# Performance work log

Measured on AMD Instinct MI355X. Metric: run time of the kernel, lower is better.

Reference implementation:

```python
import jax, jax.numpy as jnp
import numpy as np

ALPHA = 2.0   # surrogate.atan(alpha=2)
BETA = 0.9    # membrane decay
THR = 1.0     # spike threshold

@jax.custom_vjp
def atan_spike(x):
    # Heaviside forward, atan surrogate backward (snntorch convention)
    return (x > 0).astype(x.dtype)

def _atan_fwd(x):
    return atan_spike(x), x

def _atan_bwd(x, g):
    return (g * (ALPHA / 2.0) / (1.0 + (jnp.pi / 2.0 * ALPHA * x) ** 2),)

atan_spike.defvjp(_atan_fwd, _atan_bwd)


def setup_inputs() -> dict:
    key = jax.random.key(0)
    ks = jax.random.split(key, 7)
    B, T, I = 128, 128, 1024
    dims = [2048, 2048, 1024]
    x = jax.random.normal(ks[0], (B, T, I), dtype=jnp.float32)
    fan_ins = [I, dims[0], dims[1]]
    W0 = jax.random.normal(ks[1], (dims[0], fan_ins[0]), dtype=jnp.float32) / np.sqrt(fan_ins[0])
    b0 = jax.random.normal(ks[2], (dims[0],), dtype=jnp.float32) * 0.01
    W1 = jax.random.normal(ks[3], (dims[1], fan_ins[1]), dtype=jnp.float32) / np.sqrt(fan_ins[1])
    b1 = jax.random.normal(ks[4], (dims[1],), dtype=jnp.float32) * 0.01
    W2 = jax.random.normal(ks[5], (dims[2], fan_ins[2]), dtype=jnp.float32) / np.sqrt(fan_ins[2])
    b2 = jax.random.normal(ks[6], (dims[2],), dtype=jnp.float32) * 0.01
    return {"x": x, "W0": W0, "b0": b0, "W1": W1, "b1": b1, "W2": W2, "b2": b2}


def reference(x, W0, b0, W1, b1, W2, b2):
    params = ((W0, b0), (W1, b1), (W2, b2))
    B = x.shape[0]
    dims = [W0.shape[0], W1.shape[0], W2.shape[0]]
    v0 = tuple(jnp.zeros((B, d), x.dtype) for d in dims)

    def step(volts, x_t):
        h = x_t
        new_volts = []
        v = None
        for (W, b), vi in zip(params, volts):
            cur = h @ W.T + b            # [B, d]
            v = BETA * vi + cur           # leaky integration
            spk = atan_spike(v - THR)     # threshold
            v = v - spk * THR             # reset by subtraction
            new_volts.append(v)
            h = spk
        return tuple(new_volts), (h, v)

    xT = jnp.swapaxes(x, 0, 1)            # [T, B, I]
    _, (spikes, volts) = jax.lax.scan(step, v0, xT)
    # [T, B, D] -> [B, T, D]
    return jnp.swapaxes(spikes, 0, 1), jnp.swapaxes(volts, 0, 1)
```

## Files before the change

kernel.cpp:

```cpp
#include <hip/hip_runtime.h>
#include <stdint.h>


#define TT   128
#define NB   128
#define DD2  1024

#define SPK0_OFF 0u
#define SPK1_OFF (128u*128u*64u)
#define PART_OFF (2u*128u*128u*64u)
#define NHELP    192u
#define FLG_OFF  (PART_OFF + NHELP*4096u)
#define NFLG     1536u
#define WS_NEED_BYTES ((size_t)(FLG_OFF + NFLG) * 4u)

__device__ __forceinline__ void wait_ge(uint32_t* p, uint32_t tgt){
  while (__hip_atomic_load(p, __ATOMIC_ACQUIRE, __HIP_MEMORY_SCOPE_AGENT) < tgt)
    __builtin_amdgcn_s_sleep(1);
}

__device__ __forceinline__ int fswz(int k){
  return (k & 16) | ((k ^ (k >> 3)) & 12);
}

__global__ void sentinel_kernel(float* o){ o[0] = 42.0f; }

__global__ __launch_bounds__(256, 2) void snn_kernel(
    const float* __restrict__ x,
    const float* __restrict__ W0, const float* __restrict__ b0,
    const float* __restrict__ W1, const float* __restrict__ b1,
    const float* __restrict__ W2, const float* __restrict__ b2,
    float* __restrict__ out, uint32_t* __restrict__ ws)
{
  __shared__ __align__(16) float lA[128][68];
  __shared__ __align__(16) float lB[32][132];
  __shared__ uint32_t lBits[64];

  const int tid = threadIdx.x;
  const int tm  = tid & 15;
  const int tn  = tid >> 4;
  const int bid = blockIdx.x;

  uint32_t* spikes0  = ws + SPK0_OFF;
  uint32_t* spikes1  = ws + SPK1_OFF;
  float*    partials = (float*)(ws + PART_OFF);
  uint32_t* flg   = ws + FLG_OFF;
  uint32_t* pflag = flg;
  uint32_t* oflag = flg + 512;
  uint32_t* done0 = flg + 1024;
  uint32_t* done1 = flg + 1280;

  int group, kp, tl, m0, n0, K, hslot;
  const float *Wl, *bl;
  const uint32_t* spkIn; uint32_t* spkOut;
  uint32_t *dIn, *dOut;
  if (bid < 128) {
    group=0; kp=0; tl=bid;
    m0=(tl>>6)*64; n0=(tl&63)*32; K=1024; Wl=W0; bl=b0;
    spkIn=nullptr; spkOut=spikes0; dIn=nullptr; dOut=done0 + (m0>>6)*128; hslot=-1;
  } else if (bid < 384) {
    group=1; int rel=bid-128; kp=rel&1; tl=rel>>1;
    m0=(tl>>6)*64; n0=(tl&63)*32; K=2048; Wl=W1; bl=b1;
    spkIn=spikes0; spkOut=spikes1;
    dIn=done0 + (m0>>6)*128; dOut=done1 + (m0>>6)*128; hslot=tl;
  } else {
    group=2; int rel=bid-384; kp=rel&1; tl=rel>>1;
    m0=(tl>>5)*64; n0=(tl&31)*32; K=2048; Wl=W2; bl=b2;
    spkIn=spikes1; spkOut=nullptr;
    dIn=done1 + (m0>>6)*128; dOut=nullptr; hslot=128+tl;
  }
  const bool owner = (kp == 0);
  const int  K0    = kp * 1024;

  const float bias0 = bl[n0 + tn*2 + 0];
  const float bias1 = bl[n0 + tn*2 + 1];

  float vst[4][2];
  #pragma unroll
  for (int r = 0; r < 4; ++r) { vst[r][0] = 0.f; vst[r][1] = 0.f; }

  for (int t = 0; t < TT; ++t) {
    if (dIn) {
      if (tid == 0) wait_ge(&dIn[t], 64u);
      __syncthreads();
    }

    float acc2[2][4][2];
    #pragma unroll
    for (int p = 0; p < 2; ++p) {
      #pragma unroll
      for (int r = 0; r < 4; ++r) { acc2[p][r][0] = 0.f; acc2[p][r][1] = 0.f; }

      #pragma unroll 1
      for (int ch = 0; ch < 4; ++ch) {
        const int kb = K0 + p*512 + ch*128;

        #pragma unroll
        for (int it = 0; it < 4; ++it) {
          int idx = tid + it*256;
          int nrow = idx >> 5, kq = idx & 31;
          float4 w = *(const float4*)(Wl + (size_t)(n0+nrow)*K + kb + kq*4);
          *(float4*)&lB[nrow][kq*4] = w;
        }

        if (group == 0) {
          #pragma unroll
          for (int it = 0; it < 8; ++it) {
            int idx = tid + it*256;
            int mrow = idx >> 5, kq = idx & 31;
            float4 v = *(const float4*)(x + ((size_t)(m0+mrow)*TT + t)*1024 + kb + kq*4);
            int k0 = kq*4;
            lA[k0+0][mrow ^ fswz(k0+0)] = v.x;
            lA[k0+1][mrow ^ fswz(k0+1)] = v.y;
            lA[k0+2][mrow ^ fswz(k0+2)] = v.z;
            lA[k0+3][mrow ^ fswz(k0+3)] = v.w;
          }
        } else {
          const int mq   = tid & 15;
          const int sub  = tid >> 4;
          const int wsub = sub & 3;
          const int kq8  = sub >> 2;
          const size_t rb = ((size_t)t*NB + m0 + mq*4)*64 + (kb>>5) + wsub;
          uint32_t w0 = __hip_atomic_load(&spkIn[rb      ], __ATOMIC_RELAXED, __HIP_MEMORY_SCOPE_AGENT);
          uint32_t w1 = __hip_atomic_load(&spkIn[rb +  64], __ATOMIC_RELAXED, __HIP_MEMORY_SCOPE_AGENT);
          uint32_t w2 = __hip_atomic_load(&spkIn[rb + 128], __ATOMIC_RELAXED, __HIP_MEMORY_SCOPE_AGENT);
          uint32_t w3 = __hip_atomic_load(&spkIn[rb + 192], __ATOMIC_RELAXED, __HIP_MEMORY_SCOPE_AGENT);
          const int kloc = wsub*32 + kq8*8;
          #pragma unroll
          for (int i = 0; i < 8; ++i) {
            int k  = kloc + i;
            int sh = k & 31;
            float4 f;
            f.x = ((w0 >> sh) & 1u) ? 1.0f : 0.0f;
            f.y = ((w1 >> sh) & 1u) ? 1.0f : 0.0f;
            f.z = ((w2 >> sh) & 1u) ? 1.0f : 0.0f;
            f.w = ((w3 >> sh) & 1u) ? 1.0f : 0.0f;
            *(float4*)&lA[k][(mq*4) ^ fswz(k)] = f;
          }
        }
        __syncthreads();

        const float* bp0 = &lB[tn*2    ][0];
        const float* bp1 = &lB[tn*2 + 1][0];
        #pragma unroll 4
        for (int k4 = 0; k4 < 32; ++k4) {
          const int kbase = k4*4;
          const int col = (tm*4) ^ fswz(kbase);
          #pragma unroll
          for (int u = 0; u < 4; ++u) {
            const float4 a  = *(const float4*)&lA[kbase+u][col];
            const float bv0 = bp0[kbase+u];
            const float bv1 = bp1[kbase+u];
            acc2[p][0][0] = __builtin_fmaf(a.x, bv0, acc2[p][0][0]);
            acc2[p][1][0] = __builtin_fmaf(a.y, bv0, acc2[p][1][0]);
            acc2[p][2][0] = __builtin_fmaf(a.z, bv0, acc2[p][2][0]);
            acc2[p][3][0] = __builtin_fmaf(a.w, bv0, acc2[p][3][0]);
            acc2[p][0][1] = __builtin_fmaf(a.x, bv1, acc2[p][0][1]);
            acc2[p][1][1] = __builtin_fmaf(a.y, bv1, acc2[p][1][1]);
            acc2[p][2][1] = __builtin_fmaf(a.z, bv1, acc2[p][2][1]);
            acc2[p][3][1] = __builtin_fmaf(a.w, bv1, acc2[p][3][1]);
          }
        }
        __syncthreads();
      }
    }

    if (!owner) {
      if (t >= 1) { if (tid == 0) wait_ge(&oflag[bid-1], (uint32_t)t); __syncthreads(); }
      uint64_t* pb = (uint64_t*)(partials + (size_t)hslot*4096) + tid*8;
      #pragma unroll
      for (int h = 0; h < 2; ++h)
        #pragma unroll
        for (int r = 0; r < 4; ++r) {
          union { float f[2]; uint64_t u; } cv;
          cv.f[0] = acc2[h][r][0]; cv.f[1] = acc2[h][r][1];
          __hip_atomic_store(&pb[h*4+r], cv.u, __ATOMIC_RELAXED, __HIP_MEMORY_SCOPE_AGENT);
        }
      __syncthreads();
      if (tid == 0) __hip_atomic_store(&pflag[bid], (uint32_t)(t+1), __ATOMIC_RELEASE, __HIP_MEMORY_SCOPE_AGENT);
      continue;
    }

    float acc[4][2];
    #pragma unroll
    for (int r = 0; r < 4; ++r) {
      acc[r][0] = __fadd_rn(acc2[0][r][0], acc2[1][r][0]);
      acc[r][1] = __fadd_rn(acc2[0][r][1], acc2[1][r][1]);
    }

    if (hslot >= 0) {
      if (tid == 0) wait_ge(&pflag[bid+1], (uint32_t)(t+1));
      __syncthreads();
      uint64_t* pb = (uint64_t*)(partials + (size_t)hslot*4096) + tid*8;
      #pragma unroll
      for (int h = 0; h < 2; ++h)
        #pragma unroll
        for (int r = 0; r < 4; ++r) {
          union { uint64_t u; float f[2]; } cv;
          cv.u = __hip_atomic_load(&pb[h*4+r], __ATOMIC_RELAXED, __HIP_MEMORY_SCOPE_AGENT);
          acc[r][0] = __fadd_rn(acc[r][0], cv.f[0]);
          acc[r][1] = __fadd_rn(acc[r][1], cv.f[1]);
        }
      __syncthreads();
      if (tid == 0) __hip_atomic_store(&oflag[bid], (uint32_t)(t+1), __ATOMIC_RELEASE, __HIP_MEMORY_SCOPE_AGENT);
    }

    if (group < 2) { if (tid < 64) lBits[tid] = 0; __syncthreads(); }

    float sv[4][2], vv8[4][2];
    #pragma unroll
    for (int r = 0; r < 4; ++r) {
      uint32_t msk = 0;
      #pragma unroll
      for (int c = 0; c < 2; ++c) {
        float cur = __fadd_rn(acc[r][c], c ? bias1 : bias0);
        float vv  = __fadd_rn(__fmul_rn(0.9f, vst[r][c]), cur);
        float s   = (vv > 1.0f) ? 1.0f : 0.0f;
        vv = __fsub_rn(vv, s);
        vst[r][c] = vv;
        sv[r][c] = s; vv8[r][c] = vv;
        msk |= (s != 0.f) ? (1u << (tn*2 + c)) : 0u;
      }
      if (group < 2 && msk) atomicOr(&lBits[tm*4 + r], msk);
    }

    if (group == 2) {
      #pragma unroll
      for (int r = 0; r < 4; ++r) {
        size_t o  = ((size_t)(m0 + tm*4 + r)*TT + t)*DD2 + n0 + tn*2;
        *(float2*)(out + o)  = make_float2(sv[r][0], sv[r][1]);
        size_t ov = (size_t)NB*TT*DD2 + o;
        *(float2*)(out + ov) = make_float2(vv8[r][0], vv8[r][1]);
      }
    } else {
      __syncthreads();
      if (tid < 64)
        __hip_atomic_store(&spkOut[((size_t)t*NB + m0 + tid)*64 + (n0>>5)],
                           lBits[tid], __ATOMIC_RELAXED, __HIP_MEMORY_SCOPE_AGENT);
      __syncthreads();
      if (tid == 0) __hip_atomic_fetch_add(&dOut[t], 1u, __ATOMIC_RELEASE, __HIP_MEMORY_SCOPE_AGENT);
    }
  }
}

extern "C" void kernel_launch(void* const* d_in, const int* in_sizes, int n_in,
                              void* d_out, int out_size, void* d_ws, size_t ws_size,
                              hipStream_t stream) {
  (void)in_sizes; (void)n_in; (void)out_size;
  float* outf = (float*)d_out;
  if (ws_size < WS_NEED_BYTES) {
    sentinel_kernel<<<1, 1, 0, stream>>>(outf);
    return;
  }
  const float* x  = (const float*)d_in[0];
  const float* W0 = (const float*)d_in[1];
  const float* b0 = (const float*)d_in[2];
  const float* W1 = (const float*)d_in[3];
  const float* b1 = (const float*)d_in[4];
  const float* W2 = (const float*)d_in[5];
  const float* b2 = (const float*)d_in[6];
  uint32_t* ws = (uint32_t*)d_ws;

  hipMemsetAsync(ws + FLG_OFF, 0, NFLG * sizeof(uint32_t), stream);

  snn_kernel<<<512, 256, 0, stream>>>(x, W0, b0, W1, b1, W2, b2, outf, ws);
}
```

Before: 7.599 ms.

## Double-buffer LDS tiles with register prefetch, one barrier per chunk

Halves the K chunk from 128 to 64 and double-buffers the A/B shared-memory tiles. The next chunk's weights, inputs or spike words are prefetched into registers while the current chunk is computed, and the second barrier per chunk is dropped. B values are read as float4 vectors instead of scalars. The aim is to hide global-load latency behind the FMA loop and cut barrier count. The cost is more registers under launch_bounds(256,2) and a hand-placed waitcnt/barrier sequence that has to stay correct.

```diff
diff --git a/kernel.cpp b/kernel.cpp
--- a/kernel.cpp
+++ b/kernel.cpp
@@ -32,8 +32,8 @@
     const float* __restrict__ W2, const float* __restrict__ b2,
     float* __restrict__ out, uint32_t* __restrict__ ws)
 {
-  __shared__ __align__(16) float lA[128][68];
-  __shared__ __align__(16) float lB[32][132];
+  __shared__ __align__(16) float lA[2][64][68];
+  __shared__ __align__(16) float lB[2][32][68];
   __shared__ uint32_t lBits[64];
 
   const int tid = threadIdx.x;
@@ -79,6 +79,31 @@
   #pragma unroll
   for (int r = 0; r < 4; ++r) { vst[r][0] = 0.f; vst[r][1] = 0.f; }
 
+  float4   ra[4];
+  float4   rb[2];
+  uint32_t rw[4];
+
+  const int s_sub = tid >> 4;
+  const int s_kq  = tid & 15;
+
+#define LOAD_REGS(KB) do {                                                     \
+    const int kb_ = (KB);                                                      \
+    _Pragma("unroll")                                                          \
+    for (int it = 0; it < 2; ++it)                                             \
+      rb[it] = *(const float4*)(Wl + (size_t)(n0 + s_sub + it*16)*K + kb_ + s_kq*4); \
+    if (group == 0) {                                                          \
+      _Pragma("unroll")                                                        \
+      for (int it = 0; it < 4; ++it)                                           \
+        ra[it] = *(const float4*)(x + ((size_t)(m0 + s_sub + it*16)*TT + t)*1024 + kb_ + s_kq*4); \
+    } else {                                                                   \
+      const size_t base_ = ((size_t)t*NB + m0 + s_kq*4)*64 + (kb_>>5) + (s_sub>>3); \
+      _Pragma("unroll")                                                        \
+      for (int j = 0; j < 4; ++j)                                              \
+        rw[j] = __hip_atomic_load(&spkIn[base_ + (size_t)j*64],                \
+                                  __ATOMIC_RELAXED, __HIP_MEMORY_SCOPE_AGENT); \
+    }                                                                          \
+  } while (0)
+
   for (int t = 0; t < TT; ++t) {
     if (dIn) {
       if (tid == 0) wait_ge(&dIn[t], 64u);
@@ -87,70 +112,65 @@
 
     float acc2[2][4][2];
     #pragma unroll
+    for (int p = 0; p < 2; ++p)
+      #pragma unroll
+      for (int r = 0; r < 4; ++r) { acc2[p][r][0] = 0.f; acc2[p][r][1] = 0.f; }
+
+    LOAD_REGS(K0);
+
+    #pragma unroll
     for (int p = 0; p < 2; ++p) {
-      #pragma unroll
-      for (int r = 0; r < 4; ++r) { acc2[p][r][0] = 0.f; acc2[p][r][1] = 0.f; }
-
-      #pragma unroll 1
-      for (int ch = 0; ch < 4; ++ch) {
-        const int kb = K0 + p*512 + ch*128;
+      #pragma unroll 2
+      for (int ch = 0; ch < 8; ++ch) {
+        const int buf = ch & 1;
+        float (*cA)[68] = lA[buf];
+        float (*cB)[68] = lB[buf];
 
         #pragma unroll
-        for (int it = 0; it < 4; ++it) {
-          int idx = tid + it*256;
-          int nrow = idx >> 5, kq = idx & 31;
-          float4 w = *(const float4*)(Wl + (size_t)(n0+nrow)*K + kb + kq*4);
-          *(float4*)&lB[nrow][kq*4] = w;
-        }
-
+        for (int it = 0; it < 2; ++it)
+          *(float4*)&cB[s_sub + it*16][s_kq*4] = rb[it];
         if (group == 0) {
+          const int k0 = s_kq*4, sw = fswz(k0);
           #pragma unroll
-          for (int it = 0; it < 8; ++it) {
-            int idx = tid + it*256;
-            int mrow = idx >> 5, kq = idx & 31;
-            float4 v = *(const float4*)(x + ((size_t)(m0+mrow)*TT + t)*1024 + kb + kq*4);
-            int k0 = kq*4;
-            lA[k0+0][mrow ^ fswz(k0+0)] = v.x;
-            lA[k0+1][mrow ^ fswz(k0+1)] = v.y;
-            lA[k0+2][mrow ^ fswz(k0+2)] = v.z;
-            lA[k0+3][mrow ^ fswz(k0+3)] = v.w;
+          for (int it = 0; it < 4; ++it) {
+            const int col = (s_sub + it*16) ^ sw;
+            cA[k0+0][col] = ra[it].x; cA[k0+1][col] = ra[it].y;
+            cA[k0+2][col] = ra[it].z; cA[k0+3][col] = ra[it].w;
           }
         } else {
-          const int mq   = tid & 15;
-          const int sub  = tid >> 4;
-          const int wsub = sub & 3;
-          const int kq8  = sub >> 2;
-          const size_t rb = ((size_t)t*NB + m0 + mq*4)*64 + (kb>>5) + wsub;
-          uint32_t w0 = __hip_atomic_load(&spkIn[rb      ], __ATOMIC_RELAXED, __HIP_MEMORY_SCOPE_AGENT);
-          uint32_t w1 = __hip_atomic_load(&spkIn[rb +  64], __ATOMIC_RELAXED, __HIP_MEMORY_SCOPE_AGENT);
-          uint32_t w2 = __hip_atomic_load(&spkIn[rb + 128], __ATOMIC_RELAXED, __HIP_MEMORY_SCOPE_AGENT);
-          uint32_t w3 = __hip_atomic_load(&spkIn[rb + 192], __ATOMIC_RELAXED, __HIP_MEMORY_SCOPE_AGENT);
-          const int kloc = wsub*32 + kq8*8;
           #pragma unroll
-          for (int i = 0; i < 8; ++i) {
-            int k  = kloc + i;
-            int sh = k & 31;
+          for (int i = 0; i < 4; ++i) {
+            const int k  = s_sub*4 + i;
+            const int sh = k & 31;
             float4 f;
-            f.x = ((w0 >> sh) & 1u) ? 1.0f : 0.0f;
-            f.y = ((w1 >> sh) & 1u) ? 1.0f : 0.0f;
-            f.z = ((w2 >> sh) & 1u) ? 1.0f : 0.0f;
-            f.w = ((w3 >> sh) & 1u) ? 1.0f : 0.0f;
-            *(float4*)&lA[k][(mq*4) ^ fswz(k)] = f;
+            f.x = ((rw[0] >> sh) & 1u) ? 1.0f : 0.0f;
+            f.y = ((rw[1] >> sh) & 1u) ? 1.0f : 0.0f;
+            f.z = ((rw[2] >> sh) & 1u) ? 1.0f : 0.0f;
+            f.w = ((rw[3] >> sh) & 1u) ? 1.0f : 0.0f;
+            *(float4*)&cA[k][(s_kq*4) ^ fswz(k)] = f;
           }
         }
-        __syncthreads();
-
-        const float* bp0 = &lB[tn*2    ][0];
-        const float* bp1 = &lB[tn*2 + 1][0];
+
+        if (ch < 7)        LOAD_REGS(K0 + p*512 + (ch+1)*64);
+        else if (p == 0)   LOAD_REGS(K0 + 512);
+
+        __builtin_amdgcn_sched_barrier(0);
+        asm volatile("s_waitcnt lgkmcnt(0)" ::: "memory");
+        __builtin_amdgcn_s_barrier();
+        __builtin_amdgcn_sched_barrier(0);
+
         #pragma unroll 4
-        for (int k4 = 0; k4 < 32; ++k4) {
+        for (int k4 = 0; k4 < 16; ++k4) {
           const int kbase = k4*4;
-          const int col = (tm*4) ^ fswz(kbase);
+          const int sw = fswz(kbase);
+          const float* pa = &cA[kbase][(tm*4) ^ sw];
+          const float4 b0 = *(const float4*)&cB[tn*2    ][kbase];
+          const float4 b1 = *(const float4*)&cB[tn*2 + 1][kbase];
           #pragma unroll
           for (int u = 0; u < 4; ++u) {
-            const float4 a  = *(const float4*)&lA[kbase+u][col];
-            const float bv0 = bp0[kbase+u];
-            const float bv1 = bp1[kbase+u];
+            const float4 a  = *(const float4*)(pa + u*68);
+            const float bv0 = (u==0) ? b0.x : (u==1) ? b0.y : (u==2) ? b0.z : b0.w;
+            const float bv1 = (u==0) ? b1.x : (u==1) ? b1.y : (u==2) ? b1.z : b1.w;
             acc2[p][0][0] = __builtin_fmaf(a.x, bv0, acc2[p][0][0]);
             acc2[p][1][0] = __builtin_fmaf(a.y, bv0, acc2[p][1][0]);
             acc2[p][2][0] = __builtin_fmaf(a.z, bv0, acc2[p][2][0]);
@@ -161,7 +181,6 @@
             acc2[p][3][1] = __builtin_fmaf(a.w, bv1, acc2[p][3][1]);
           }
         }
-        __syncthreads();
       }
     }
 
@@ -241,6 +260,7 @@
       if (tid == 0) __hip_atomic_fetch_add(&dOut[t], 1u, __ATOMIC_RELEASE, __HIP_MEMORY_SCOPE_AGENT);
     }
   }
+#undef LOAD_REGS
 }
 
 extern "C" void kernel_launch(void* const* d_in, const int* in_sizes, int n_in,
```

Result: slower. 10.09 ms (+32.7%).

## Merge split-K block pairs into 512-thread blocks with LDS partial reduction

Applied to the files above, without the earlier changes.

Each pair of split-K blocks for layers 1 and 2 becomes one 512-thread block. The two halves exchange partial sums through shared memory and a barrier, instead of through global partial buffers guarded by per-block flags. Layer-0 blocks now each handle two tiles, and the done-counter targets are adjusted to match the new block counts. The inner loop also reads the weight tile as float4 instead of scalar loads. The cost is doubled shared memory per block, so fewer blocks fit on each CU.

```diff
diff --git a/kernel.cpp b/kernel.cpp
--- a/kernel.cpp
+++ b/kernel.cpp
@@ -19,58 +19,56 @@
     __builtin_amdgcn_s_sleep(1);
 }
 
-__device__ __forceinline__ int fswz(int k){
+__device__ __forceinline__ constexpr int fswz(int k){
   return (k & 16) | ((k ^ (k >> 3)) & 12);
 }
 
 __global__ void sentinel_kernel(float* o){ o[0] = 42.0f; }
 
-__global__ __launch_bounds__(256, 2) void snn_kernel(
+__global__ __launch_bounds__(512, 2) void snn_kernel(
     const float* __restrict__ x,
     const float* __restrict__ W0, const float* __restrict__ b0,
     const float* __restrict__ W1, const float* __restrict__ b1,
     const float* __restrict__ W2, const float* __restrict__ b2,
     float* __restrict__ out, uint32_t* __restrict__ ws)
 {
-  __shared__ __align__(16) float lA[128][68];
-  __shared__ __align__(16) float lB[32][132];
-  __shared__ uint32_t lBits[64];
-
-  const int tid = threadIdx.x;
-  const int tm  = tid & 15;
-  const int tn  = tid >> 4;
-  const int bid = blockIdx.x;
-
-  uint32_t* spikes0  = ws + SPK0_OFF;
-  uint32_t* spikes1  = ws + SPK1_OFF;
-  float*    partials = (float*)(ws + PART_OFF);
+  __shared__ __align__(16) float lA[2][128][68];
+  __shared__ __align__(16) float lB[2][32][132];
+  __shared__ uint32_t lBits2[2][64];
+
+  const int tid  = threadIdx.x;
+  const int h    = tid >> 8;
+  const int t256 = tid & 255;
+  const int tm   = t256 & 15;
+  const int tn   = t256 >> 4;
+  const int bid  = blockIdx.x;
+
+  uint32_t* spikes0 = ws + SPK0_OFF;
+  uint32_t* spikes1 = ws + SPK1_OFF;
   uint32_t* flg   = ws + FLG_OFF;
-  uint32_t* pflag = flg;
-  uint32_t* oflag = flg + 512;
   uint32_t* done0 = flg + 1024;
   uint32_t* done1 = flg + 1280;
 
-  int group, kp, tl, m0, n0, K, hslot;
+  int group, tl, m0, n0, K, K0, dTgt;
   const float *Wl, *bl;
   const uint32_t* spkIn; uint32_t* spkOut;
   uint32_t *dIn, *dOut;
-  if (bid < 128) {
-    group=0; kp=0; tl=bid;
-    m0=(tl>>6)*64; n0=(tl&63)*32; K=1024; Wl=W0; bl=b0;
-    spkIn=nullptr; spkOut=spikes0; dIn=nullptr; dOut=done0 + (m0>>6)*128; hslot=-1;
-  } else if (bid < 384) {
-    group=1; int rel=bid-128; kp=rel&1; tl=rel>>1;
-    m0=(tl>>6)*64; n0=(tl&63)*32; K=2048; Wl=W1; bl=b1;
+  if (bid < 64) {
+    group=0; tl=bid*2+h;
+    m0=(tl>>6)*64; n0=(tl&63)*32; K=1024; K0=0; Wl=W0; bl=b0;
+    spkIn=nullptr; spkOut=spikes0; dIn=nullptr; dOut=done0+(m0>>6)*128; dTgt=0;
+  } else if (bid < 192) {
+    group=1; tl=bid-64;
+    m0=(tl>>6)*64; n0=(tl&63)*32; K=2048; K0=h*1024; Wl=W1; bl=b1;
     spkIn=spikes0; spkOut=spikes1;
-    dIn=done0 + (m0>>6)*128; dOut=done1 + (m0>>6)*128; hslot=tl;
+    dIn=done0+(m0>>6)*128; dOut=done1+(m0>>6)*128; dTgt=32;
   } else {
-    group=2; int rel=bid-384; kp=rel&1; tl=rel>>1;
-    m0=(tl>>5)*64; n0=(tl&31)*32; K=2048; Wl=W2; bl=b2;
+    group=2; tl=bid-192;
+    m0=(tl>>5)*64; n0=(tl&31)*32; K=2048; K0=h*1024; Wl=W2; bl=b2;
     spkIn=spikes1; spkOut=nullptr;
-    dIn=done1 + (m0>>6)*128; dOut=nullptr; hslot=128+tl;
+    dIn=done1+(m0>>6)*128; dOut=nullptr; dTgt=64;
   }
-  const bool owner = (kp == 0);
-  const int  K0    = kp * 1024;
+  const bool own = (group == 0) || (h == 0);
 
   const float bias0 = bl[n0 + tn*2 + 0];
   const float bias1 = bl[n0 + tn*2 + 1];
@@ -79,78 +77,85 @@
   #pragma unroll
   for (int r = 0; r < 4; ++r) { vst[r][0] = 0.f; vst[r][1] = 0.f; }
 
+  const int e_mq   = t256 & 15;
+  const int e_sub  = t256 >> 4;
+  const int e_wsub = e_sub & 3;
+  const int e_kq8  = e_sub >> 2;
+  const int e_kloc = e_wsub*32 + e_kq8*8;
+
+  float (*cA)[68]  = lA[h];
+  float (*cB)[132] = lB[h];
+
   for (int t = 0; t < TT; ++t) {
     if (dIn) {
-      if (tid == 0) wait_ge(&dIn[t], 64u);
+      if (tid == 0) wait_ge(&dIn[t], (uint32_t)dTgt);
       __syncthreads();
     }
 
     float acc2[2][4][2];
     #pragma unroll
-    for (int p = 0; p < 2; ++p) {
+    for (int p = 0; p < 2; ++p)
       #pragma unroll
       for (int r = 0; r < 4; ++r) { acc2[p][r][0] = 0.f; acc2[p][r][1] = 0.f; }
 
+    #pragma unroll
+    for (int p = 0; p < 2; ++p) {
       #pragma unroll 1
       for (int ch = 0; ch < 4; ++ch) {
         const int kb = K0 + p*512 + ch*128;
 
         #pragma unroll
         for (int it = 0; it < 4; ++it) {
-          int idx = tid + it*256;
+          int idx = t256 + it*256;
           int nrow = idx >> 5, kq = idx & 31;
           float4 w = *(const float4*)(Wl + (size_t)(n0+nrow)*K + kb + kq*4);
-          *(float4*)&lB[nrow][kq*4] = w;
+          *(float4*)&cB[nrow][kq*4] = w;
         }
 
         if (group == 0) {
           #pragma unroll
           for (int it = 0; it < 8; ++it) {
-            int idx = tid + it*256;
+            int idx = t256 + it*256;
             int mrow = idx >> 5, kq = idx & 31;
             float4 v = *(const float4*)(x + ((size_t)(m0+mrow)*TT + t)*1024 + kb + kq*4);
             int k0 = kq*4;
-            lA[k0+0][mrow ^ fswz(k0+0)] = v.x;
-            lA[k0+1][mrow ^ fswz(k0+1)] = v.y;
-            lA[k0+2][mrow ^ fswz(k0+2)] = v.z;
-            lA[k0+3][mrow ^ fswz(k0+3)] = v.w;
+            lA[h][k0+0][mrow ^ fswz(k0+0)] = v.x;
+            lA[h][k0+1][mrow ^ fswz(k0+1)] = v.y;
+            lA[h][k0+2][mrow ^ fswz(k0+2)] = v.z;
+            lA[h][k0+3][mrow ^ fswz(k0+3)] = v.w;
           }
         } else {
-          const int mq   = tid & 15;
-          const int sub  = tid >> 4;
-          const int wsub = sub & 3;
-          const int kq8  = sub >> 2;
-          const size_t rb = ((size_t)t*NB + m0 + mq*4)*64 + (kb>>5) + wsub;
-          uint32_t w0 = __hip_atomic_load(&spkIn[rb      ], __ATOMIC_RELAXED, __HIP_MEMORY_SCOPE_AGENT);
-          uint32_t w1 = __hip_atomic_load(&spkIn[rb +  64], __ATOMIC_RELAXED, __HIP_MEMORY_SCOPE_AGENT);
-          uint32_t w2 = __hip_atomic_load(&spkIn[rb + 128], __ATOMIC_RELAXED, __HIP_MEMORY_SCOPE_AGENT);
-          uint32_t w3 = __hip_atomic_load(&spkIn[rb + 192], __ATOMIC_RELAXED, __HIP_MEMORY_SCOPE_AGENT);
-          const int kloc = wsub*32 + kq8*8;
+          const size_t rbase = ((size_t)t*NB + m0 + e_mq*4)*64 + (kb>>5) + e_wsub;
+          uint32_t w0 = __hip_atomic_load(&spkIn[rbase      ], __ATOMIC_RELAXED, __HIP_MEMORY_SCOPE_AGENT);
+          uint32_t w1 = __hip_atomic_load(&spkIn[rbase +  64], __ATOMIC_RELAXED, __HIP_MEMORY_SCOPE_AGENT);
+          uint32_t w2 = __hip_atomic_load(&spkIn[rbase + 128], __ATOMIC_RELAXED, __HIP_MEMORY_SCOPE_AGENT);
+          uint32_t w3 = __hip_atomic_load(&spkIn[rbase + 192], __ATOMIC_RELAXED, __HIP_MEMORY_SCOPE_AGENT);
           #pragma unroll
           for (int i = 0; i < 8; ++i) {
-            int k  = kloc + i;
+            int k  = e_kloc + i;
             int sh = k & 31;
             float4 f;
             f.x = ((w0 >> sh) & 1u) ? 1.0f : 0.0f;
             f.y = ((w1 >> sh) & 1u) ? 1.0f : 0.0f;
             f.z = ((w2 >> sh) & 1u) ? 1.0f : 0.0f;
             f.w = ((w3 >> sh) & 1u) ? 1.0f : 0.0f;
-            *(float4*)&lA[k][(mq*4) ^ fswz(k)] = f;
+            *(float4*)&cA[k][(e_mq*4) ^ fswz(k)] = f;
           }
         }
         __syncthreads();
 
-        const float* bp0 = &lB[tn*2    ][0];
-        const float* bp1 = &lB[tn*2 + 1][0];
         #pragma unroll 4
         for (int k4 = 0; k4 < 32; ++k4) {
           const int kbase = k4*4;
-          const int col = (tm*4) ^ fswz(kbase);
+          const int sw = fswz(kbase);
+          const float* pa = &cA[kbase][(tm*4) ^ sw];
+          const float4 b0v = *(const float4*)&cB[tn*2    ][kbase];
+          const float4 b1v = *(const float4*)&cB[tn*2 + 1][kbase];
           #pragma unroll
           for (int u = 0; u < 4; ++u) {
-            const float4 a  = *(const float4*)&lA[kbase+u][col];
-            const float bv0 = bp0[kbase+u];
-            const float bv1 = bp1[kbase+u];
+            const float4 a  = *(const float4*)(pa + u*68);
+            const float bv0 = (u==0) ? b0v.x : (u==1) ? b0v.y : (u==2) ? b0v.z : b0v.w;
+            const float bv1 = (u==0) ? b1v.x : (u==1) ? b1v.y : (u==2) ? b1v.z : b1v.w;
             acc2[p][0][0] = __builtin_fmaf(a.x, bv0, acc2[p][0][0]);
             acc2[p][1][0] = __builtin_fmaf(a.y, bv0, acc2[p][1][0]);
             acc2[p][2][0] = __builtin_fmaf(a.z, bv0, acc2[p][2][0]);
@@ -165,22 +170,6 @@
       }
     }
 
-    if (!owner) {
-      if (t >= 1) { if (tid == 0) wait_ge(&oflag[bid-1], (uint32_t)t); __syncthreads(); }
-      uint64_t* pb = (uint64_t*)(partials + (size_t)hslot*4096) + tid*8;
-      #pragma unroll
-      for (int h = 0; h < 2; ++h)
-        #pragma unroll
-        for (int r = 0; r < 4; ++r) {
-          union { float f[2]; uint64_t u; } cv;
-          cv.f[0] = acc2[h][r][0]; cv.f[1] = acc2[h][r][1];
-          __hip_atomic_store(&pb[h*4+r], cv.u, __ATOMIC_RELAXED, __HIP_MEMORY_SCOPE_AGENT);
-        }
-      __syncthreads();
-      if (tid == 0) __hip_atomic_store(&pflag[bid], (uint32_t)(t+1), __ATOMIC_RELEASE, __HIP_MEMORY_SCOPE_AGENT);
-      continue;
-    }
-
     float acc[4][2];
     #pragma unroll
     for (int r = 0; r < 4; ++r) {
@@ -188,55 +177,64 @@
       acc[r][1] = __fadd_rn(acc2[0][r][1], acc2[1][r][1]);
     }
 
-    if (hslot >= 0) {
-      if (tid == 0) wait_ge(&pflag[bid+1], (uint32_t)(t+1));
-      __syncthreads();
-      uint64_t* pb = (uint64_t*)(partials + (size_t)hslot*4096) + tid*8;
-      #pragma unroll
-      for (int h = 0; h < 2; ++h)
-        #pragma unroll
-        for (int r = 0; r < 4; ++r) {
-          union { uint64_t u; float f[2]; } cv;
-          cv.u = __hip_atomic_load(&pb[h*4+r], __ATOMIC_RELAXED, __HIP_MEMORY_SCOPE_AGENT);
-          acc[r][0] = __fadd_rn(acc[r][0], cv.f[0]);
-          acc[r][1] = __fadd_rn(acc[r][1], cv.f[1]);
-        }
-      __syncthreads();
-      if (tid == 0) __hip_atomic_store(&oflag[bid], (uint32_t)(t+1), __ATOMIC_RELEASE, __HIP_MEMORY_SCOPE_AGENT);
-    }
-
-    if (group < 2) { if (tid < 64) lBits[tid] = 0; __syncthreads(); }
-
-    float sv[4][2], vv8[4][2];
-    #pragma unroll
-    for (int r = 0; r < 4; ++r) {
-      uint32_t msk = 0;
-      #pragma unroll
-      for (int c = 0; c < 2; ++c) {
-        float cur = __fadd_rn(acc[r][c], c ? bias1 : bias0);
-        float vv  = __fadd_rn(__fmul_rn(0.9f, vst[r][c]), cur);
-        float s   = (vv > 1.0f) ? 1.0f : 0.0f;
-        vv = __fsub_rn(vv, s);
-        vst[r][c] = vv;
-        sv[r][c] = s; vv8[r][c] = vv;
-        msk |= (s != 0.f) ? (1u << (tn*2 + c)) : 0u;
-      }
-      if (group < 2 && msk) atomicOr(&lBits[tm*4 + r], msk);
-    }
-
-    if (group == 2) {
+    if (group != 0) {
+      float* ex = &lA[1][0][0];
+      if (h == 1) {
+        #pragma unroll
+        for (int q = 0; q < 4; ++q) {
+          const int hh = q >> 1, rb = (q & 1) * 2;
+          *(float4*)&ex[t256*16 + q*4] = make_float4(
+              acc2[hh][rb+0][0], acc2[hh][rb+0][1],
+              acc2[hh][rb+1][0], acc2[hh][rb+1][1]);
+        }
+      }
+      __syncthreads();
+      if (h == 0) {
+        #pragma unroll
+        for (int hh = 0; hh < 2; ++hh)
+          #pragma unroll
+          for (int r = 0; r < 4; ++r) {
+            acc[r][0] = __fadd_rn(acc[r][0], ex[t256*16 + hh*8 + r*2 + 0]);
+            acc[r][1] = __fadd_rn(acc[r][1], ex[t256*16 + hh*8 + r*2 + 1]);
+          }
+      }
+    }
+
+    if (group < 2) { if (t256 < 64) lBits2[h][t256] = 0; __syncthreads(); }
+
+    if (own) {
+      float sv[4][2], vv8[4][2];
       #pragma unroll
       for (int r = 0; r < 4; ++r) {
-        size_t o  = ((size_t)(m0 + tm*4 + r)*TT + t)*DD2 + n0 + tn*2;
-        *(float2*)(out + o)  = make_float2(sv[r][0], sv[r][1]);
-        size_t ov = (size_t)NB*TT*DD2 + o;
-        *(float2*)(out + ov) = make_float2(vv8[r][0], vv8[r][1]);
-      }
-    } else {
-      __syncthreads();
-      if (tid < 64)
-        __hip_atomic_store(&spkOut[((size_t)t*NB + m0 + tid)*64 + (n0>>5)],
-                           lBits[tid], __ATOMIC_RELAXED, __HIP_MEMORY_SCOPE_AGENT);
+        uint32_t msk = 0;
+        #pragma unroll
+        for (int c = 0; c < 2; ++c) {
+          float cur = __fadd_rn(acc[r][c], c ? bias1 : bias0);
+          float vv  = __fadd_rn(__fmul_rn(0.9f, vst[r][c]), cur);
+          float s   = (vv > 1.0f) ? 1.0f : 0.0f;
+          vv = __fsub_rn(vv, s);
+          vst[r][c] = vv;
+          sv[r][c] = s; vv8[r][c] = vv;
+          msk |= (s != 0.f) ? (1u << (tn*2 + c)) : 0u;
+        }
+        if (group < 2 && msk) atomicOr(&lBits2[h][tm*4 + r], msk);
+      }
+      if (group == 2) {
+        #pragma unroll
+        for (int r = 0; r < 4; ++r) {
+          size_t o  = ((size_t)(m0 + tm*4 + r)*TT + t)*DD2 + n0 + tn*2;
+          *(float2*)(out + o)  = make_float2(sv[r][0], sv[r][1]);
+          size_t ov = (size_t)NB*TT*DD2 + o;
+          *(float2*)(out + ov) = make_float2(vv8[r][0], vv8[r][1]);
+        }
+      }
+    }
+
+    if (group < 2) {
+      __syncthreads();
+      if (own && t256 < 64)
+        __hip_atomic_store(&spkOut[((size_t)t*NB + m0 + t256)*64 + (n0>>5)],
+                           lBits2[h][t256], __ATOMIC_RELAXED, __HIP_MEMORY_SCOPE_AGENT);
       __syncthreads();
       if (tid == 0) __hip_atomic_fetch_add(&dOut[t], 1u, __ATOMIC_RELEASE, __HIP_MEMORY_SCOPE_AGENT);
     }
@@ -263,5 +261,5 @@
 
   hipMemsetAsync(ws + FLG_OFF, 0, NFLG * sizeof(uint32_t), stream);
 
-  snn_kernel<<<512, 256, 0, stream>>>(x, W0, b0, W1, b1, W2, b2, outf, ws);
-}
+  snn_kernel<<<256, 512, 0, stream>>>(x, W0, b0, W1, b1, W2, b2, outf, ws);
+}
```

New measurement: 7.061 ms. 7.1% less time.

## Widen tiles to 64 columns with 512 threads and split K four ways

Applied to the files above, without the earlier changes.

Each block now uses 512 threads and a 64x64 output tile instead of 32 columns. The reduction dimension is split across 2 (layer 0) or 4 (layers 1 and 2) blocks, each covering 512 of K. The owner block waits for all helper partials and sums them, and flag and partial-slot layouts plus the spike-bit packing are reworked to match. The aim is shorter per-block K loops and more reuse of each loaded activation tile, which shortens the serial per-timestep chain. The cost is more partial-sum traffic through global memory, more flag waits per step, and heavier register and LDS use per block.

```diff
diff --git a/kernel.cpp b/kernel.cpp
--- a/kernel.cpp
+++ b/kernel.cpp
@@ -9,9 +9,9 @@
 #define SPK0_OFF 0u
 #define SPK1_OFF (128u*128u*64u)
 #define PART_OFF (2u*128u*128u*64u)
-#define NHELP    192u
+#define NHELP    352u
 #define FLG_OFF  (PART_OFF + NHELP*4096u)
-#define NFLG     1536u
+#define NFLG     1280u
 #define WS_NEED_BYTES ((size_t)(FLG_OFF + NFLG) * 4u)
 
 __device__ __forceinline__ void wait_ge(uint32_t* p, uint32_t tgt){
@@ -19,13 +19,13 @@
     __builtin_amdgcn_s_sleep(1);
 }
 
-__device__ __forceinline__ int fswz(int k){
+__device__ __forceinline__ constexpr int fswz(int k){
   return (k & 16) | ((k ^ (k >> 3)) & 12);
 }
 
 __global__ void sentinel_kernel(float* o){ o[0] = 42.0f; }
 
-__global__ __launch_bounds__(256, 2) void snn_kernel(
+__global__ __launch_bounds__(512, 4) void snn_kernel(
     const float* __restrict__ x,
     const float* __restrict__ W0, const float* __restrict__ b0,
     const float* __restrict__ W1, const float* __restrict__ b1,
@@ -33,8 +33,8 @@
     float* __restrict__ out, uint32_t* __restrict__ ws)
 {
   __shared__ __align__(16) float lA[128][68];
-  __shared__ __align__(16) float lB[32][132];
-  __shared__ uint32_t lBits[64];
+  __shared__ __align__(16) float lB[64][132];
+  __shared__ uint32_t lBits[128];
 
   const int tid = threadIdx.x;
   const int tm  = tid & 15;
@@ -46,31 +46,35 @@
   float*    partials = (float*)(ws + PART_OFF);
   uint32_t* flg   = ws + FLG_OFF;
   uint32_t* pflag = flg;
-  uint32_t* oflag = flg + 512;
-  uint32_t* done0 = flg + 1024;
-  uint32_t* done1 = flg + 1280;
-
-  int group, kp, tl, m0, n0, K, hslot;
+  uint32_t* oflag = flg + 352;
+  uint32_t* done0 = flg + 544;
+  uint32_t* done1 = flg + 800;
+
+  int group, pairk, tl, m0, n0, K, ksp, hslot, ownerid;
   const float *Wl, *bl;
   const uint32_t* spkIn; uint32_t* spkOut;
   uint32_t *dIn, *dOut;
   if (bid < 128) {
-    group=0; kp=0; tl=bid;
-    m0=(tl>>6)*64; n0=(tl&63)*32; K=1024; Wl=W0; bl=b0;
-    spkIn=nullptr; spkOut=spikes0; dIn=nullptr; dOut=done0 + (m0>>6)*128; hslot=-1;
+    group=0; ksp=2; pairk=bid&1; tl=bid>>1;
+    m0=(tl>>5)*64; n0=(tl&31)*64; K=1024; Wl=W0; bl=b0;
+    spkIn=nullptr; spkOut=spikes0;
+    dIn=nullptr; dOut=done0+(m0>>6)*128;
+    hslot = tl; ownerid = tl;
   } else if (bid < 384) {
-    group=1; int rel=bid-128; kp=rel&1; tl=rel>>1;
-    m0=(tl>>6)*64; n0=(tl&63)*32; K=2048; Wl=W1; bl=b1;
+    group=1; ksp=4; int rel=bid-128; pairk=rel&3; tl=rel>>2;
+    m0=(tl>>5)*64; n0=(tl&31)*64; K=2048; Wl=W1; bl=b1;
     spkIn=spikes0; spkOut=spikes1;
-    dIn=done0 + (m0>>6)*128; dOut=done1 + (m0>>6)*128; hslot=tl;
+    dIn=done0+(m0>>6)*128; dOut=done1+(m0>>6)*128;
+    hslot = 64 + tl*3 + (pairk-1); ownerid = 64 + tl;
   } else {
-    group=2; int rel=bid-384; kp=rel&1; tl=rel>>1;
-    m0=(tl>>5)*64; n0=(tl&31)*32; K=2048; Wl=W2; bl=b2;
+    group=2; ksp=4; int rel=bid-384; pairk=rel&3; tl=rel>>2;
+    m0=(tl>>4)*64; n0=(tl&15)*64; K=2048; Wl=W2; bl=b2;
     spkIn=spikes1; spkOut=nullptr;
-    dIn=done1 + (m0>>6)*128; dOut=nullptr; hslot=128+tl;
+    dIn=done1+(m0>>6)*128; dOut=nullptr;
+    hslot = 256 + tl*3 + (pairk-1); ownerid = 128 + tl;
   }
-  const bool owner = (kp == 0);
-  const int  K0    = kp * 1024;
+  const bool owner = (pairk == 0);
+  const int  K0    = pairk * 512;
 
   const float bias0 = bl[n0 + tn*2 + 0];
   const float bias1 = bl[n0 + tn*2 + 1];
@@ -79,133 +83,127 @@
   #pragma unroll
   for (int r = 0; r < 4; ++r) { vst[r][0] = 0.f; vst[r][1] = 0.f; }
 
+  const int e_q  = tid & 15;
+  const int e_g  = tid >> 4;
+  const int e_w  = e_g >> 3;
+  const int e_sh = (e_g & 7) * 4;
+
   for (int t = 0; t < TT; ++t) {
     if (dIn) {
-      if (tid == 0) wait_ge(&dIn[t], 64u);
-      __syncthreads();
-    }
-
-    float acc2[2][4][2];
-    #pragma unroll
-    for (int p = 0; p < 2; ++p) {
-      #pragma unroll
-      for (int r = 0; r < 4; ++r) { acc2[p][r][0] = 0.f; acc2[p][r][1] = 0.f; }
-
-      #pragma unroll 1
-      for (int ch = 0; ch < 4; ++ch) {
-        const int kb = K0 + p*512 + ch*128;
-
-        #pragma unroll
-        for (int it = 0; it < 4; ++it) {
-          int idx = tid + it*256;
-          int nrow = idx >> 5, kq = idx & 31;
-          float4 w = *(const float4*)(Wl + (size_t)(n0+nrow)*K + kb + kq*4);
-          *(float4*)&lB[nrow][kq*4] = w;
-        }
-
-        if (group == 0) {
-          #pragma unroll
-          for (int it = 0; it < 8; ++it) {
-            int idx = tid + it*256;
-            int mrow = idx >> 5, kq = idx & 31;
-            float4 v = *(const float4*)(x + ((size_t)(m0+mrow)*TT + t)*1024 + kb + kq*4);
-            int k0 = kq*4;
-            lA[k0+0][mrow ^ fswz(k0+0)] = v.x;
-            lA[k0+1][mrow ^ fswz(k0+1)] = v.y;
-            lA[k0+2][mrow ^ fswz(k0+2)] = v.z;
-            lA[k0+3][mrow ^ fswz(k0+3)] = v.w;
-          }
-        } else {
-          const int mq   = tid & 15;
-          const int sub  = tid >> 4;
-          const int wsub = sub & 3;
-          const int kq8  = sub >> 2;
-          const size_t rb = ((size_t)t*NB + m0 + mq*4)*64 + (kb>>5) + wsub;
-          uint32_t w0 = __hip_atomic_load(&spkIn[rb      ], __ATOMIC_RELAXED, __HIP_MEMORY_SCOPE_AGENT);
-          uint32_t w1 = __hip_atomic_load(&spkIn[rb +  64], __ATOMIC_RELAXED, __HIP_MEMORY_SCOPE_AGENT);
-          uint32_t w2 = __hip_atomic_load(&spkIn[rb + 128], __ATOMIC_RELAXED, __HIP_MEMORY_SCOPE_AGENT);
-          uint32_t w3 = __hip_atomic_load(&spkIn[rb + 192], __ATOMIC_RELAXED, __HIP_MEMORY_SCOPE_AGENT);
-          const int kloc = wsub*32 + kq8*8;
-          #pragma unroll
-          for (int i = 0; i < 8; ++i) {
-            int k  = kloc + i;
-            int sh = k & 31;
-            float4 f;
-            f.x = ((w0 >> sh) & 1u) ? 1.0f : 0.0f;
-            f.y = ((w1 >> sh) & 1u) ? 1.0f : 0.0f;
-            f.z = ((w2 >> sh) & 1u) ? 1.0f : 0.0f;
-            f.w = ((w3 >> sh) & 1u) ? 1.0f : 0.0f;
-            *(float4*)&lA[k][(mq*4) ^ fswz(k)] = f;
-          }
-        }
-        __syncthreads();
-
-        const float* bp0 = &lB[tn*2    ][0];
-        const float* bp1 = &lB[tn*2 + 1][0];
-        #pragma unroll 4
-        for (int k4 = 0; k4 < 32; ++k4) {
-          const int kbase = k4*4;
-          const int col = (tm*4) ^ fswz(kbase);
-          #pragma unroll
-          for (int u = 0; u < 4; ++u) {
-            const float4 a  = *(const float4*)&lA[kbase+u][col];
-            const float bv0 = bp0[kbase+u];
-            const float bv1 = bp1[kbase+u];
-            acc2[p][0][0] = __builtin_fmaf(a.x, bv0, acc2[p][0][0]);
-            acc2[p][1][0] = __builtin_fmaf(a.y, bv0, acc2[p][1][0]);
-            acc2[p][2][0] = __builtin_fmaf(a.z, bv0, acc2[p][2][0]);
-            acc2[p][3][0] = __builtin_fmaf(a.w, bv0, acc2[p][3][0]);
-            acc2[p][0][1] = __builtin_fmaf(a.x, bv1, acc2[p][0][1]);
-            acc2[p][1][1] = __builtin_fmaf(a.y, bv1, acc2[p][1][1]);
-            acc2[p][2][1] = __builtin_fmaf(a.z, bv1, acc2[p][2][1]);
-            acc2[p][3][1] = __builtin_fmaf(a.w, bv1, acc2[p][3][1]);
-          }
-        }
-        __syncthreads();
-      }
-    }
-
-    if (!owner) {
-      if (t >= 1) { if (tid == 0) wait_ge(&oflag[bid-1], (uint32_t)t); __syncthreads(); }
-      uint64_t* pb = (uint64_t*)(partials + (size_t)hslot*4096) + tid*8;
-      #pragma unroll
-      for (int h = 0; h < 2; ++h)
-        #pragma unroll
-        for (int r = 0; r < 4; ++r) {
-          union { float f[2]; uint64_t u; } cv;
-          cv.f[0] = acc2[h][r][0]; cv.f[1] = acc2[h][r][1];
-          __hip_atomic_store(&pb[h*4+r], cv.u, __ATOMIC_RELAXED, __HIP_MEMORY_SCOPE_AGENT);
-        }
-      __syncthreads();
-      if (tid == 0) __hip_atomic_store(&pflag[bid], (uint32_t)(t+1), __ATOMIC_RELEASE, __HIP_MEMORY_SCOPE_AGENT);
-      continue;
+      if (tid == 0) wait_ge(&dIn[t], 32u);
+      __syncthreads();
     }
 
     float acc[4][2];
     #pragma unroll
-    for (int r = 0; r < 4; ++r) {
-      acc[r][0] = __fadd_rn(acc2[0][r][0], acc2[1][r][0]);
-      acc[r][1] = __fadd_rn(acc2[0][r][1], acc2[1][r][1]);
-    }
-
-    if (hslot >= 0) {
-      if (tid == 0) wait_ge(&pflag[bid+1], (uint32_t)(t+1));
-      __syncthreads();
-      uint64_t* pb = (uint64_t*)(partials + (size_t)hslot*4096) + tid*8;
-      #pragma unroll
-      for (int h = 0; h < 2; ++h)
+    for (int r = 0; r < 4; ++r) { acc[r][0] = 0.f; acc[r][1] = 0.f; }
+
+    #pragma unroll 1
+    for (int ch = 0; ch < 4; ++ch) {
+      const int kb = K0 + ch*128;
+
+      #pragma unroll
+      for (int it = 0; it < 4; ++it) {
+        int idx = tid + it*512;
+        int nrow = idx >> 5, kq = idx & 31;
+        float4 w = *(const float4*)(Wl + (size_t)(n0+nrow)*K + kb + kq*4);
+        *(float4*)&lB[nrow][kq*4] = w;
+      }
+
+      if (group == 0) {
+        #pragma unroll
+        for (int it = 0; it < 4; ++it) {
+          int idx = tid + it*512;
+          int mrow = idx >> 5, kq = idx & 31;
+          float4 v = *(const float4*)(x + ((size_t)(m0+mrow)*TT + t)*1024 + kb + kq*4);
+          int k0 = kq*4;
+          const int sw = fswz(k0);
+          const int col = mrow ^ sw;
+          lA[k0+0][col] = v.x; lA[k0+1][col] = v.y;
+          lA[k0+2][col] = v.z; lA[k0+3][col] = v.w;
+        }
+      } else {
+        const size_t rbase = ((size_t)t*NB + m0 + e_q*4)*64 + (kb>>5) + e_w;
+        uint32_t w0 = __hip_atomic_load(&spkIn[rbase      ], __ATOMIC_RELAXED, __HIP_MEMORY_SCOPE_AGENT);
+        uint32_t w1 = __hip_atomic_load(&spkIn[rbase +  64], __ATOMIC_RELAXED, __HIP_MEMORY_SCOPE_AGENT);
+        uint32_t w2 = __hip_atomic_load(&spkIn[rbase + 128], __ATOMIC_RELAXED, __HIP_MEMORY_SCOPE_AGENT);
+        uint32_t w3 = __hip_atomic_load(&spkIn[rbase + 192], __ATOMIC_RELAXED, __HIP_MEMORY_SCOPE_AGENT);
+        #pragma unroll
+        for (int j = 0; j < 4; ++j) {
+          const int k  = e_g*4 + j;
+          const int sh = e_sh + j;
+          float4 f;
+          f.x = ((w0 >> sh) & 1u) ? 1.0f : 0.0f;
+          f.y = ((w1 >> sh) & 1u) ? 1.0f : 0.0f;
+          f.z = ((w2 >> sh) & 1u) ? 1.0f : 0.0f;
+          f.w = ((w3 >> sh) & 1u) ? 1.0f : 0.0f;
+          *(float4*)&lA[k][(e_q*4) ^ fswz(k)] = f;
+        }
+      }
+      __syncthreads();
+
+      #pragma unroll 4
+      for (int k4 = 0; k4 < 32; ++k4) {
+        const int kbase = k4*4;
+        const int sw = fswz(kbase);
+        const float* pa = &lA[kbase][(tm*4) ^ sw];
+        const float4 q0 = *(const float4*)&lB[tn*2    ][kbase];
+        const float4 q1 = *(const float4*)&lB[tn*2 + 1][kbase];
+        #pragma unroll
+        for (int u = 0; u < 4; ++u) {
+          const float4 a  = *(const float4*)(pa + u*68);
+          const float b0v = (u==0) ? q0.x : (u==1) ? q0.y : (u==2) ? q0.z : q0.w;
+          const float b1v = (u==0) ? q1.x : (u==1) ? q1.y : (u==2) ? q1.z : q1.w;
+          acc[0][0] = __builtin_fmaf(a.x, b0v, acc[0][0]);
+          acc[1][0] = __builtin_fmaf(a.y, b0v, acc[1][0]);
+          acc[2][0] = __builtin_fmaf(a.z, b0v, acc[2][0]);
+          acc[3][0] = __builtin_fmaf(a.w, b0v, acc[3][0]);
+          acc[0][1] = __builtin_fmaf(a.x, b1v, acc[0][1]);
+          acc[1][1] = __builtin_fmaf(a.y, b1v, acc[1][1]);
+          acc[2][1] = __builtin_fmaf(a.z, b1v, acc[2][1]);
+          acc[3][1] = __builtin_fmaf(a.w, b1v, acc[3][1]);
+        }
+      }
+      __syncthreads();
+    }
+
+    if (!owner) {
+      if (t >= 1) { if (tid == 0) wait_ge(&oflag[ownerid], (uint32_t)t); __syncthreads(); }
+      uint64_t* pb = (uint64_t*)(partials + (size_t)hslot*4096) + tid*4;
+      #pragma unroll
+      for (int r = 0; r < 4; ++r) {
+        union { float f[2]; uint64_t u; } cv;
+        cv.f[0] = acc[r][0]; cv.f[1] = acc[r][1];
+        __hip_atomic_store(&pb[r], cv.u, __ATOMIC_RELAXED, __HIP_MEMORY_SCOPE_AGENT);
+      }
+      __syncthreads();
+      if (tid == 0) __hip_atomic_store(&pflag[hslot], (uint32_t)(t+1), __ATOMIC_RELEASE, __HIP_MEMORY_SCOPE_AGENT);
+      continue;
+    }
+
+    {
+      if (tid == 0)
+        for (int p = 1; p < ksp; ++p) {
+          int hs = (group==0) ? tl : ((group==1) ? (64 + tl*3 + (p-1)) : (256 + tl*3 + (p-1)));
+          wait_ge(&pflag[hs], (uint32_t)(t+1));
+        }
+      __syncthreads();
+      for (int p = 1; p < ksp; ++p) {
+        int hs = (group==0) ? tl : ((group==1) ? (64 + tl*3 + (p-1)) : (256 + tl*3 + (p-1)));
+        uint64_t* pb = (uint64_t*)(partials + (size_t)hs*4096) + tid*4;
         #pragma unroll
         for (int r = 0; r < 4; ++r) {
           union { uint64_t u; float f[2]; } cv;
-          cv.u = __hip_atomic_load(&pb[h*4+r], __ATOMIC_RELAXED, __HIP_MEMORY_SCOPE_AGENT);
+          cv.u = __hip_atomic_load(&pb[r], __ATOMIC_RELAXED, __HIP_MEMORY_SCOPE_AGENT);
           acc[r][0] = __fadd_rn(acc[r][0], cv.f[0]);
           acc[r][1] = __fadd_rn(acc[r][1], cv.f[1]);
         }
-      __syncthreads();
-      if (tid == 0) __hip_atomic_store(&oflag[bid], (uint32_t)(t+1), __ATOMIC_RELEASE, __HIP_MEMORY_SCOPE_AGENT);
-    }
-
-    if (group < 2) { if (tid < 64) lBits[tid] = 0; __syncthreads(); }
+      }
+      __syncthreads();
+      if (tid == 0) __hip_atomic_store(&oflag[ownerid], (uint32_t)(t+1), __ATOMIC_RELEASE, __HIP_MEMORY_SCOPE_AGENT);
+    }
+
+    if (group < 2) { if (tid < 128) lBits[tid] = 0; __syncthreads(); }
 
     float sv[4][2], vv8[4][2];
     #pragma unroll
@@ -219,9 +217,9 @@
         vv = __fsub_rn(vv, s);
         vst[r][c] = vv;
         sv[r][c] = s; vv8[r][c] = vv;
-        msk |= (s != 0.f) ? (1u << (tn*2 + c)) : 0u;
-      }
-      if (group < 2 && msk) atomicOr(&lBits[tm*4 + r], msk);
+        msk |= (s != 0.f) ? (1u << ((tn*2 + c) & 31)) : 0u;
+      }
+      if (group < 2 && msk) atomicOr(&lBits[(tm*4 + r)*2 + (tn>>4)], msk);
     }
 
     if (group == 2) {
@@ -234,8 +232,8 @@
       }
     } else {
       __syncthreads();
-      if (tid < 64)
-        __hip_atomic_store(&spkOut[((size_t)t*NB + m0 + tid)*64 + (n0>>5)],
+      if (tid < 128)
+        __hip_atomic_store(&spkOut[((size_t)t*NB + m0 + (tid>>1))*64 + (n0>>5) + (tid&1)],
                            lBits[tid], __ATOMIC_RELAXED, __HIP_MEMORY_SCOPE_AGENT);
       __syncthreads();
       if (tid == 0) __hip_atomic_fetch_add(&dOut[t], 1u, __ATOMIC_RELEASE, __HIP_MEMORY_SCOPE_AGENT);
@@ -263,5 +261,5 @@
 
   hipMemsetAsync(ws + FLG_OFF, 0, NFLG * sizeof(uint32_t), stream);
 
-  snn_kernel<<<512, 256, 0, stream>>>(x, W0, b0, W1, b1, W2, b2, outf, ws);
-}
+  snn_kernel<<<512, 512, 0, stream>>>(x, W0, b0, W1, b1, W2, b2, outf, ws);
+}
```

After: 8.476 ms. 11.5% more time.
